# Kernel tuning notes

Measured on AMD Instinct MI355X. Metric: run time of the kernel, lower is better.

## Reference

```python
import jax, jax.numpy as jnp
import numpy as np

K_SIZE = 5  # local patch size


def extract_patches(x, k):
    """im2col-style k x k patch extraction with SAME zero padding.
    x: [B,H,W,C] -> [B,H,W,k*k,C]"""
    B, H, W, C = x.shape
    pad = k // 2
    xp = jnp.pad(x, ((0, 0), (pad, pad), (pad, pad), (0, 0)))
    # loop over fixed k*k offsets (25), stacked along a new patch axis
    slices = [xp[:, i:i + H, j:j + W, :] for i in range(k) for j in range(k)]
    return jnp.stack(slices, axis=3)  # [B,H,W,k*k,C]


def setup_inputs() -> dict:
    key = jax.random.key(0)
    k1, k2, k3 = jax.random.split(key, 3)
    B, H, W, C, BIN = 2, 128, 128, 64, 64
    return {
        "main": jax.random.normal(k1, (B, H, W, C), dtype=jnp.float32),
        "ref": jax.random.normal(k2, (B, H, W, C), dtype=jnp.float32),
        "ref_value": jax.random.normal(k3, (B, H, W, BIN), dtype=jnp.float32),
    }


def reference(main, ref, ref_value):
    k = K_SIZE
    ref_stacked = extract_patches(ref, k)            # [B,H,W,k*k,C]
    ref_value_stacked = extract_patches(ref_value, k)  # [B,H,W,k*k,BIN]
    # dot-product attention over the k*k patch axis
    scores = jnp.einsum('bhwpc,bhwc->bhwp', ref_stacked, main)  # [B,H,W,k*k]
    attn = jax.nn.softmax(scores, axis=3)
    # attention-weighted sum of value patches
    out = jnp.einsum('bhwp,bhwpv->bhwv', attn, ref_value_stacked)  # [B,H,W,BIN]
    return out
```

## Files before the change

### kernel.cpp

```cpp
#include <hip/hip_runtime.h>


#define BB 2
#define HH 128
#define WW 128
#define CC 64
#define KK 5

template <int CTRL>
__device__ __forceinline__ float dpp_add(float v) {
    int r = __builtin_amdgcn_update_dpp(0, __float_as_int(v), CTRL, 0xF, 0xF, true);
    return v + __int_as_float(r);
}

__device__ __forceinline__ float group16_sum(float v) {
    v = dpp_add<0xB1>(v);
    v = dpp_add<0x4E>(v);
    v = dpp_add<0x124>(v);
    v = dpp_add<0x128>(v);
    return v;
}

__global__ __launch_bounds__(256, 4) void local_attn_kernel(
    const float* __restrict__ mainp,
    const float* __restrict__ refp,
    const float* __restrict__ refvp,
    float* __restrict__ outp)
{
    const int tid    = threadIdx.x;
    const int lane16 = tid & 15;
    const int pix    = tid >> 4;
    const int seg    = blockIdx.x;
    const int wseg   = seg & 7;
    const int h      = (seg >> 3) & (HH - 1);
    const int b      = seg >> 10;
    const int w      = wseg * 16 + pix;
    const int cb     = lane16 * 4;

    const size_t pbase = (((size_t)(b * HH + h)) * WW + w) * CC + cb;
    const float4 m4 = *reinterpret_cast<const float4*>(mainp + pbase);

    float sc[KK * KK];

    #pragma unroll
    for (int di = 0; di < KK; ++di) {
        const int hh  = h + di - 2;
        const int hhc = min(max(hh, 0), HH - 1);
        const float* rrow = refp + ((size_t)(b * HH + hhc) * WW) * CC + cb;
        #pragma unroll
        for (int dj = 0; dj < KK; ++dj) {
            const int ww  = w + dj - 2;
            const int wwc = min(max(ww, 0), WW - 1);
            const float4 r4 =
                *reinterpret_cast<const float4*>(rrow + (size_t)wwc * CC);
            const bool ok = ((unsigned)hh < (unsigned)HH) &
                            ((unsigned)ww < (unsigned)WW);
            const float p = m4.x * r4.x + m4.y * r4.y + m4.z * r4.z + m4.w * r4.w;
            sc[di * KK + dj] = ok ? p : 0.0f;
        }
    }

    #pragma unroll
    for (int p = 0; p < KK * KK; ++p) sc[p] = group16_sum(sc[p]);

    float mx = sc[0];
    #pragma unroll
    for (int p = 1; p < KK * KK; ++p) mx = fmaxf(mx, sc[p]);
    float s = 0.0f;
    #pragma unroll
    for (int p = 0; p < KK * KK; ++p) { sc[p] = __expf(sc[p] - mx); s += sc[p]; }
    const float inv = 1.0f / s;
    #pragma unroll
    for (int p = 0; p < KK * KK; ++p) sc[p] *= inv;

    float4 acc = make_float4(0.f, 0.f, 0.f, 0.f);
    #pragma unroll
    for (int di = 0; di < KK; ++di) {
        const int hh  = h + di - 2;
        const int hhc = min(max(hh, 0), HH - 1);
        const float* vrow = refvp + ((size_t)(b * HH + hhc) * WW) * CC + cb;
        #pragma unroll
        for (int dj = 0; dj < KK; ++dj) {
            const int ww  = w + dj - 2;
            const int wwc = min(max(ww, 0), WW - 1);
            const float4 v4 =
                *reinterpret_cast<const float4*>(vrow + (size_t)wwc * CC);
            const bool ok = ((unsigned)hh < (unsigned)HH) &
                            ((unsigned)ww < (unsigned)WW);
            const float a = ok ? sc[di * KK + dj] : 0.0f;
            acc.x += a * v4.x;
            acc.y += a * v4.y;
            acc.z += a * v4.z;
            acc.w += a * v4.w;
        }
    }

    *reinterpret_cast<float4*>(outp + pbase) = acc;
}

extern "C" void kernel_launch(void* const* d_in, const int* in_sizes, int n_in,
                              void* d_out, int out_size, void* d_ws, size_t ws_size,
                              hipStream_t stream) {
    const float* mainp = (const float*)d_in[0];
    const float* refp  = (const float*)d_in[1];
    const float* refvp = (const float*)d_in[2];
    float* outp        = (float*)d_out;

    const int blocks = BB * HH * (WW / 16);
    local_attn_kernel<<<blocks, 256, 0, stream>>>(mainp, refp, refvp, outp);
}
```

Measured before the change: 84.40 us.

## Stage 5x20 ref and value halo tiles in LDS, reuse across pixels

Each block now cooperatively loads a zero-padded 5-row by 20-column neighbourhood tile (25.6 KB) of the ref tensor into shared memory, computes scores from it, then reloads the same tile buffer with ref_value for the weighted sum. This replaces 25 redundant global/L2 float4 loads per pixel per tensor with roughly 6.25 loads per pixel, and removes per-tap bounds checks. The cost is three extra block barriers, serialization between the ref and value phases since one buffer is reused, and LDS usage that may limit occupancy to a few blocks per CU.

```diff
diff --git a/kernel.cpp b/kernel.cpp
--- a/kernel.cpp
+++ b/kernel.cpp
@@ -6,6 +6,9 @@
 #define WW 128
 #define CC 64
 #define KK 5
+#define PAD 2
+#define TC 20
+#define NV (KK * TC)
 
 template <int CTRL>
 __device__ __forceinline__ float dpp_add(float v) {
@@ -21,12 +24,42 @@
     return v;
 }
 
+__device__ __forceinline__ void stage_tile(const float* __restrict__ src,
+                                           float* __restrict__ lds,
+                                           int b, int h, int w0,
+                                           int grp, int lane16) {
+    #pragma unroll
+    for (int i = 0; i < 7; ++i) {
+        const int v = grp + 16 * i;
+        if (v < NV) {
+            const int r   = v / TC;
+            const int c   = v - r * TC;
+            const int hg  = h + r - PAD;
+            const int wg  = w0 + c - PAD;
+            const int hgc = min(max(hg, 0), HH - 1);
+            const int wgc = min(max(wg, 0), WW - 1);
+            const float4 d = *reinterpret_cast<const float4*>(
+                src + (((size_t)(b * HH + hgc)) * WW + wgc) * CC + lane16 * 4);
+            const bool ok = ((unsigned)hg < (unsigned)HH) &
+                            ((unsigned)wg < (unsigned)WW);
+            float4 z;
+            z.x = ok ? d.x : 0.0f;
+            z.y = ok ? d.y : 0.0f;
+            z.z = ok ? d.z : 0.0f;
+            z.w = ok ? d.w : 0.0f;
+            *reinterpret_cast<float4*>(lds + (size_t)v * CC + lane16 * 4) = z;
+        }
+    }
+}
+
 __global__ __launch_bounds__(256, 4) void local_attn_kernel(
     const float* __restrict__ mainp,
     const float* __restrict__ refp,
     const float* __restrict__ refvp,
     float* __restrict__ outp)
 {
+    __shared__ float tile[NV * CC];
+
     const int tid    = threadIdx.x;
     const int lane16 = tid & 15;
     const int pix    = tid >> 4;
@@ -34,29 +67,26 @@
     const int wseg   = seg & 7;
     const int h      = (seg >> 3) & (HH - 1);
     const int b      = seg >> 10;
-    const int w      = wseg * 16 + pix;
+    const int w0     = wseg * 16;
+    const int w      = w0 + pix;
     const int cb     = lane16 * 4;
 
     const size_t pbase = (((size_t)(b * HH + h)) * WW + w) * CC + cb;
     const float4 m4 = *reinterpret_cast<const float4*>(mainp + pbase);
 
+    stage_tile(refp, tile, b, h, w0, pix, lane16);
+    __syncthreads();
+
+    const float* tbase = tile + (size_t)pix * CC + cb;
+
     float sc[KK * KK];
-
     #pragma unroll
-    for (int di = 0; di < KK; ++di) {
-        const int hh  = h + di - 2;
-        const int hhc = min(max(hh, 0), HH - 1);
-        const float* rrow = refp + ((size_t)(b * HH + hhc) * WW) * CC + cb;
+    for (int r = 0; r < KK; ++r) {
         #pragma unroll
         for (int dj = 0; dj < KK; ++dj) {
-            const int ww  = w + dj - 2;
-            const int wwc = min(max(ww, 0), WW - 1);
-            const float4 r4 =
-                *reinterpret_cast<const float4*>(rrow + (size_t)wwc * CC);
-            const bool ok = ((unsigned)hh < (unsigned)HH) &
-                            ((unsigned)ww < (unsigned)WW);
-            const float p = m4.x * r4.x + m4.y * r4.y + m4.z * r4.z + m4.w * r4.w;
-            sc[di * KK + dj] = ok ? p : 0.0f;
+            const float4 t =
+                *reinterpret_cast<const float4*>(tbase + (r * TC + dj) * CC);
+            sc[r * KK + dj] = m4.x * t.x + m4.y * t.y + m4.z * t.z + m4.w * t.w;
         }
     }
 
@@ -73,25 +103,22 @@
     #pragma unroll
     for (int p = 0; p < KK * KK; ++p) sc[p] *= inv;
 
+    __syncthreads();
+    stage_tile(refvp, tile, b, h, w0, pix, lane16);
+    __syncthreads();
+
     float4 acc = make_float4(0.f, 0.f, 0.f, 0.f);
     #pragma unroll
-    for (int di = 0; di < KK; ++di) {
-        const int hh  = h + di - 2;
-        const int hhc = min(max(hh, 0), HH - 1);
-        const float* vrow = refvp + ((size_t)(b * HH + hhc) * WW) * CC + cb;
+    for (int r = 0; r < KK; ++r) {
         #pragma unroll
         for (int dj = 0; dj < KK; ++dj) {
-            const int ww  = w + dj - 2;
-            const int wwc = min(max(ww, 0), WW - 1);
-            const float4 v4 =
-                *reinterpret_cast<const float4*>(vrow + (size_t)wwc * CC);
-            const bool ok = ((unsigned)hh < (unsigned)HH) &
-                            ((unsigned)ww < (unsigned)WW);
-            const float a = ok ? sc[di * KK + dj] : 0.0f;
-            acc.x += a * v4.x;
-            acc.y += a * v4.y;
-            acc.z += a * v4.z;
-            acc.w += a * v4.w;
+            const float4 t =
+                *reinterpret_cast<const float4*>(tbase + (r * TC + dj) * CC);
+            const float a = sc[r * KK + dj];
+            acc.x += a * t.x;
+            acc.y += a * t.y;
+            acc.z += a * t.z;
+            acc.w += a * t.w;
         }
     }
 
```

New measurement: 82.89 us. About the same (-1.8%).
